# Kernel optimization log

Hardware: AMD Instinct MI355X
Metric: run time of the kernel (lower is better)

## Reference

```python
import jax, jax.numpy as jnp
import numpy as np

LOG_2PI = float(np.log(2.0 * np.pi))


def setup_inputs() -> dict:
    key = jax.random.key(0)
    k1, k2, k3 = jax.random.split(key, 3)
    B, T, F, K = 16, 1024, 1024, 500
    X = jax.random.normal(k1, (B, T, F), dtype=jnp.float32)
    mu = jax.random.normal(k2, (K, F), dtype=jnp.float32)
    # cov must be positive for log(cov); uniform in [0.5, 1.5)
    cov = jax.random.uniform(k3, (K, F), dtype=jnp.float32) + 0.5
    return {"X": X, "mu": mu, "cov": cov}


def reference(X, mu, cov):
    # Diagonal-covariance GMM log-likelihoods: out[b,t,k] = log N(X[b,t]; mu[k], diag(cov[k]))
    # Algebraic expansion of 0.5*sum((x-mu)^2/cov) into two GEMMs + bias, avoiding
    # the BxTxKxF broadcast intermediate. Same math as the torch module.
    D = mu.shape[-1]
    inv_cov = 1.0 / cov                                   # (K, F)
    C = -0.5 * D * LOG_2PI - 0.5 * jnp.sum(jnp.log(cov), axis=-1)  # (K,)
    quad = jnp.einsum('btf,kf->btk', X * X, inv_cov)      # sum x^2/cov
    cross = jnp.einsum('btf,kf->btk', X, mu * inv_cov)    # sum x*mu/cov
    const = jnp.sum(mu * mu * inv_cov, axis=-1)           # (K,) sum mu^2/cov
    ULL = 0.5 * (quad - 2.0 * cross + const[None, None, :])
    return C[None, None, :] - ULL                         # (B, T, K)
```

## Files before the change

### kernel.cpp

```cpp
#include <hip/hip_runtime.h>
#include <hip/hip_bf16.h>


typedef __attribute__((ext_vector_type(8))) __bf16 bf16x8;
typedef __attribute__((ext_vector_type(4))) float  f32x4;

#define LOG_2PI 1.837877066409345339082f

constexpr int M_TOT = 16384;
constexpr int F_DIM = 1024;
constexpr int K_GMM = 500;
constexpr int N_PAD = 512;

constexpr int BM  = 128;
constexpr int BN  = 128;
constexpr int BKF = 32;
constexpr int NIT = F_DIM / BKF;

__device__ __forceinline__ void gload_lds16(const void* g, void* l) {
    __builtin_amdgcn_global_load_lds(
        (const __attribute__((address_space(1))) unsigned*)g,
        (__attribute__((address_space(3))) unsigned*)l, 16, 0, 0);
}

__device__ __forceinline__ unsigned pack_sq_x(float x) {
    __hip_bfloat162 h = __float22bfloat162_rn(make_float2(x * x, x));
    union { __hip_bfloat162 h; unsigned u; } cv;
    cv.h = h;
    return cv.u;
}

__global__ __launch_bounds__(256) void prep_w_kernel(
    const float* __restrict__ mu, const float* __restrict__ cov,
    unsigned* __restrict__ Wimg, float* __restrict__ bias)
{
    const int k = blockIdx.x;
    const int t = threadIdx.x;
    const int r  = k & 127;
    const int tt = k >> 7;
    const int rsw = r & 7;
    float sl = 0.f, sq = 0.f;
    #pragma unroll
    for (int j = 0; j < 4; ++j) {
        const int f  = t + j * 256;
        const int it = f >> 5;
        const int cc = (f >> 2) & 7;
        const int q  = f & 3;
        const int dw = (tt * 32 + it) * 4096 + r * 32 + ((cc ^ rsw) << 2) + q;
        if (k < K_GMM) {
            const float c = cov[k * F_DIM + f];
            const float m = mu[k * F_DIM + f];
            const float ic = 1.0f / c;
            __hip_bfloat162 h = __float22bfloat162_rn(make_float2(-0.5f * ic, m * ic));
            union { __hip_bfloat162 h; unsigned u; } cv; cv.h = h;
            Wimg[dw] = cv.u;
            sl += logf(c);
            sq += m * m * ic;
        } else {
            Wimg[dw] = 0u;
        }
    }
    #pragma unroll
    for (int off = 32; off > 0; off >>= 1) {
        sl += __shfl_down(sl, off, 64);
        sq += __shfl_down(sq, off, 64);
    }
    __shared__ float red[8];
    if ((t & 63) == 0) { red[(t >> 6) * 2] = sl; red[(t >> 6) * 2 + 1] = sq; }
    __syncthreads();
    if (t == 0) {
        const float SL = red[0] + red[2] + red[4] + red[6];
        const float SQ = red[1] + red[3] + red[5] + red[7];
        bias[k] = (k < K_GMM)
                ? (-0.5f * (F_DIM * LOG_2PI) - 0.5f * SL - 0.5f * SQ) : 0.f;
    }
}

__global__ __launch_bounds__(256, 2) void gemm_kernel(
    const float* __restrict__ X, const unsigned* __restrict__ Wimg,
    const float* __restrict__ bias, float* __restrict__ out)
{
    __shared__ __align__(16) char smem[65536];
    float* ep = reinterpret_cast<float*>(smem);

    const int bid    = blockIdx.x;
    const int m_base = (bid & 127) * BM;
    const int n_tile = bid >> 7;
    const int n_base = n_tile * BN;

    const int tid  = threadIdx.x;
    const int lane = tid & 63;
    const int wv   = tid >> 6;
    const int wr   = (wv >> 1) * 64;
    const int wc   = (wv & 1) * 64;
    const int hi   = lane >> 4;
    const int lo   = lane & 15;
    const int lsw  = lo & 7;

    const int sr = tid >> 1;
    const int sh = tid & 1;

    const float4* Xv   = reinterpret_cast<const float4*>(X);
    const char*   Wimc = reinterpret_cast<const char*>(Wimg);

    f32x4 acc[4][4];
    #pragma unroll
    for (int a = 0; a < 4; ++a)
        #pragma unroll
        for (int b = 0; b < 4; ++b)
            acc[a][b] = (f32x4){0.f, 0.f, 0.f, 0.f};

    {
        const char* g0 = Wimc + (size_t)(n_tile * 32 + 0) * 16384;
        #pragma unroll
        for (int i = 0; i < 4; ++i)
            gload_lds16(g0 + i * 4096 + wv * 1024 + lane * 16,
                        smem + 32768 + i * 4096 + wv * 1024);
        float4 a0[4];
        #pragma unroll
        for (int j = 0; j < 4; ++j)
            a0[j] = Xv[(m_base + sr) * (F_DIM / 4) + sh * 4 + j];
        unsigned short* A0 = reinterpret_cast<unsigned short*>(smem);
        #pragma unroll
        for (int j = 0; j < 4; ++j) {
            const int chunk = (sh * 4 + j) ^ (sr & 7);
            uint4 wa;
            wa.x = pack_sq_x(a0[j].x);
            wa.y = pack_sq_x(a0[j].y);
            wa.z = pack_sq_x(a0[j].z);
            wa.w = pack_sq_x(a0[j].w);
            *reinterpret_cast<uint4*>(&A0[sr * 64 + chunk * 8]) = wa;
        }
    }
    __syncthreads();

    for (int it = 0; it < NIT; ++it) {
        const int cur = it & 1;
        const int nxt = cur ^ 1;
        const unsigned short* Asc =
            reinterpret_cast<const unsigned short*>(smem + cur * 16384);
        const unsigned short* Bsc =
            reinterpret_cast<const unsigned short*>(smem + 32768 + cur * 16384);
        char*           Bdst = smem + 32768 + nxt * 16384;
        unsigned short* Adst = reinterpret_cast<unsigned short*>(smem + nxt * 16384);

        float4 a_next[4];
        if (it + 1 < NIT) {
            const char* gs = Wimc + (size_t)(n_tile * 32 + it + 1) * 16384;
            #pragma unroll
            for (int i = 0; i < 4; ++i)
                gload_lds16(gs + i * 4096 + wv * 1024 + lane * 16,
                            Bdst + i * 4096 + wv * 1024);
            #pragma unroll
            for (int j = 0; j < 4; ++j)
                a_next[j] = Xv[(m_base + sr) * (F_DIM / 4) + (it + 1) * 8 + sh * 4 + j];
        }

        #pragma unroll
        for (int c = 0; c < 2; ++c) {
            bf16x8 af[4], bf[4];
            #pragma unroll
            for (int a = 0; a < 4; ++a) {
                const int row   = wr + a * 16 + lo;
                const int chunk = (c * 4 + hi) ^ lsw;
                af[a] = *reinterpret_cast<const bf16x8*>(&Asc[row * 64 + chunk * 8]);
            }
            #pragma unroll
            for (int b = 0; b < 4; ++b) {
                const int row   = wc + b * 16 + lo;
                const int chunk = (c * 4 + hi) ^ lsw;
                bf[b] = *reinterpret_cast<const bf16x8*>(&Bsc[row * 64 + chunk * 8]);
            }
            #pragma unroll
            for (int a = 0; a < 4; ++a)
                #pragma unroll
                for (int b = 0; b < 4; ++b)
                    acc[a][b] = __builtin_amdgcn_mfma_f32_16x16x32_bf16(
                        af[a], bf[b], acc[a][b], 0, 0, 0);
        }

        if (it + 1 < NIT) {
            #pragma unroll
            for (int j = 0; j < 4; ++j) {
                const int chunk = (sh * 4 + j) ^ (sr & 7);
                uint4 wa;
                wa.x = pack_sq_x(a_next[j].x);
                wa.y = pack_sq_x(a_next[j].y);
                wa.z = pack_sq_x(a_next[j].z);
                wa.w = pack_sq_x(a_next[j].w);
                *reinterpret_cast<uint4*>(&Adst[sr * 64 + chunk * 8]) = wa;
            }
        }
        __syncthreads();
    }

    const int ncols = (K_GMM - n_base < BN) ? (K_GMM - n_base) : BN;
    #pragma unroll
    for (int p = 0; p < 2; ++p) {
        __syncthreads();
        if ((wv >> 1) == p) {
            #pragma unroll
            for (int b = 0; b < 4; ++b) {
                const int col = wc + b * 16 + lo;
                const float bv = bias[n_base + col];
                #pragma unroll
                for (int a = 0; a < 4; ++a)
                    #pragma unroll
                    for (int i = 0; i < 4; ++i)
                        ep[(a * 16 + hi * 4 + i) * 128 + col] = acc[a][b][i] + bv;
            }
        }
        __syncthreads();
        #pragma unroll
        for (int k = 0; k < 8; ++k) {
            const int f    = k * 256 + tid;
            const int row  = f >> 5;
            const int slot = f & 31;
            if (slot * 4 < ncols) {
                const float4 v = *reinterpret_cast<const float4*>(&ep[row * 128 + slot * 4]);
                *reinterpret_cast<float4*>(
                    &out[(size_t)(m_base + p * 64 + row) * K_GMM + n_base + slot * 4]) = v;
            }
        }
    }
}

extern "C" void kernel_launch(void* const* d_in, const int* in_sizes, int n_in,
                              void* d_out, int out_size, void* d_ws, size_t ws_size,
                              hipStream_t stream)
{
    (void)in_sizes; (void)n_in; (void)out_size; (void)ws_size;
    const float* X   = (const float*)d_in[0];
    const float* mu  = (const float*)d_in[1];
    const float* cov = (const float*)d_in[2];
    float* out = (float*)d_out;

    unsigned* Wimg = (unsigned*)d_ws;
    float*    bias = (float*)((char*)d_ws + (size_t)N_PAD * F_DIM * 4);

    prep_w_kernel<<<dim3(N_PAD), dim3(256), 0, stream>>>(mu, cov, Wimg, bias);
    gemm_kernel<<<dim3((M_TOT / BM) * (N_PAD / BN)), dim3(256), 0, stream>>>(X, Wimg, bias, out);
}
```

Baseline: 57.82 us.

## Deepen GEMM pipeline with triple-buffered B tiles and explicit waitcnt barriers

The GEMM main loop is restructured so the weight tiles are triple-buffered in LDS (80KB) and prefetched two iterations ahead. X rows alternate between two register buffers, and the loop is unrolled by two. The implicit __syncthreads is replaced by manual s_waitcnt vmcnt(8)/lgkmcnt(0) plus s_barrier and sched_barrier, which lets one stage's loads stay in flight across the barrier. The aim is to hide global-load latency better; the cost is more LDS per block and fragile hand-counted waitcnt logic.

New measurement: 54.60 us. 1.06x faster.

```diff
diff --git a/kernel.cpp b/kernel.cpp
--- a/kernel.cpp
+++ b/kernel.cpp
@@ -80,7 +80,7 @@
     const float* __restrict__ X, const unsigned* __restrict__ Wimg,
     const float* __restrict__ bias, float* __restrict__ out)
 {
-    __shared__ __align__(16) char smem[65536];
+    __shared__ __align__(16) char smem[81920];
     float* ep = reinterpret_cast<float*>(smem);
 
     const int bid    = blockIdx.x;
@@ -110,52 +110,36 @@
         for (int b = 0; b < 4; ++b)
             acc[a][b] = (f32x4){0.f, 0.f, 0.f, 0.f};
 
-    {
-        const char* g0 = Wimc + (size_t)(n_tile * 32 + 0) * 16384;
+    auto stageB = [&](int itS, int bufS) {
+        const char* gs = Wimc + (size_t)(n_tile * 32 + itS) * 16384;
         #pragma unroll
         for (int i = 0; i < 4; ++i)
-            gload_lds16(g0 + i * 4096 + wv * 1024 + lane * 16,
-                        smem + 32768 + i * 4096 + wv * 1024);
-        float4 a0[4];
+            gload_lds16(gs + i * 4096 + wv * 1024 + lane * 16,
+                        smem + 32768 + bufS * 16384 + i * 4096 + wv * 1024);
+    };
+    auto loadA = [&](int itS, float4* ar) {
         #pragma unroll
         for (int j = 0; j < 4; ++j)
-            a0[j] = Xv[(m_base + sr) * (F_DIM / 4) + sh * 4 + j];
-        unsigned short* A0 = reinterpret_cast<unsigned short*>(smem);
+            ar[j] = Xv[(m_base + sr) * (F_DIM / 4) + itS * 8 + sh * 4 + j];
+    };
+    auto packA = [&](const float4* ar, int ab) {
+        unsigned short* Ad = reinterpret_cast<unsigned short*>(smem + ab * 16384);
         #pragma unroll
         for (int j = 0; j < 4; ++j) {
             const int chunk = (sh * 4 + j) ^ (sr & 7);
             uint4 wa;
-            wa.x = pack_sq_x(a0[j].x);
-            wa.y = pack_sq_x(a0[j].y);
-            wa.z = pack_sq_x(a0[j].z);
-            wa.w = pack_sq_x(a0[j].w);
-            *reinterpret_cast<uint4*>(&A0[sr * 64 + chunk * 8]) = wa;
-        }
-    }
-    __syncthreads();
-
-    for (int it = 0; it < NIT; ++it) {
-        const int cur = it & 1;
-        const int nxt = cur ^ 1;
+            wa.x = pack_sq_x(ar[j].x);
+            wa.y = pack_sq_x(ar[j].y);
+            wa.z = pack_sq_x(ar[j].z);
+            wa.w = pack_sq_x(ar[j].w);
+            *reinterpret_cast<uint4*>(&Ad[sr * 64 + chunk * 8]) = wa;
+        }
+    };
+    auto compute = [&](int ab, int bb) {
         const unsigned short* Asc =
-            reinterpret_cast<const unsigned short*>(smem + cur * 16384);
+            reinterpret_cast<const unsigned short*>(smem + ab * 16384);
         const unsigned short* Bsc =
-            reinterpret_cast<const unsigned short*>(smem + 32768 + cur * 16384);
-        char*           Bdst = smem + 32768 + nxt * 16384;
-        unsigned short* Adst = reinterpret_cast<unsigned short*>(smem + nxt * 16384);
-
-        float4 a_next[4];
-        if (it + 1 < NIT) {
-            const char* gs = Wimc + (size_t)(n_tile * 32 + it + 1) * 16384;
-            #pragma unroll
-            for (int i = 0; i < 4; ++i)
-                gload_lds16(gs + i * 4096 + wv * 1024 + lane * 16,
-                            Bdst + i * 4096 + wv * 1024);
-            #pragma unroll
-            for (int j = 0; j < 4; ++j)
-                a_next[j] = Xv[(m_base + sr) * (F_DIM / 4) + (it + 1) * 8 + sh * 4 + j];
-        }
-
+            reinterpret_cast<const unsigned short*>(smem + 32768 + bb * 16384);
         #pragma unroll
         for (int c = 0; c < 2; ++c) {
             bf16x8 af[4], bf[4];
@@ -178,26 +162,49 @@
                     acc[a][b] = __builtin_amdgcn_mfma_f32_16x16x32_bf16(
                         af[a], bf[b], acc[a][b], 0, 0, 0);
         }
-
-        if (it + 1 < NIT) {
-            #pragma unroll
-            for (int j = 0; j < 4; ++j) {
-                const int chunk = (sh * 4 + j) ^ (sr & 7);
-                uint4 wa;
-                wa.x = pack_sq_x(a_next[j].x);
-                wa.y = pack_sq_x(a_next[j].y);
-                wa.z = pack_sq_x(a_next[j].z);
-                wa.w = pack_sq_x(a_next[j].w);
-                *reinterpret_cast<uint4*>(&Adst[sr * 64 + chunk * 8]) = wa;
-            }
-        }
-        __syncthreads();
+    };
+
+    float4 aA[4], aB[4];
+    stageB(0, 0);
+    loadA(0, aB);
+    stageB(1, 1);
+    loadA(1, aA);
+    packA(aB, 0);
+    asm volatile("s_waitcnt vmcnt(8) lgkmcnt(0)" ::: "memory");
+    __builtin_amdgcn_s_barrier();
+    __builtin_amdgcn_sched_barrier(0);
+
+    for (int it = 0; it < NIT; it += 2) {
+        const int b0 = it % 3;
+        const int b1 = (it + 1) % 3;
+        const int b2 = (it + 2) % 3;
+        const int b3 = (it + 3) % 3;
+
+        if (it + 2 < NIT) { stageB(it + 2, b2); loadA(it + 2, aB); }
+        compute(0, b0);
+        packA(aA, 1);
+        if (it + 2 < NIT)
+            asm volatile("s_waitcnt vmcnt(8) lgkmcnt(0)" ::: "memory");
+        else
+            asm volatile("s_waitcnt vmcnt(0) lgkmcnt(0)" ::: "memory");
+        __builtin_amdgcn_s_barrier();
+        __builtin_amdgcn_sched_barrier(0);
+
+        if (it + 3 < NIT) { stageB(it + 3, b3); loadA(it + 3, aA); }
+        compute(1, b1);
+        if (it + 2 < NIT) packA(aB, 0);
+        if (it + 3 < NIT)
+            asm volatile("s_waitcnt vmcnt(8) lgkmcnt(0)" ::: "memory");
+        else
+            asm volatile("s_waitcnt vmcnt(0) lgkmcnt(0)" ::: "memory");
+        __builtin_amdgcn_s_barrier();
+        __builtin_amdgcn_sched_barrier(0);
     }
 
     const int ncols = (K_GMM - n_base < BN) ? (K_GMM - n_base) : BN;
     #pragma unroll
     for (int p = 0; p < 2; ++p) {
-        __syncthreads();
+        if (p) __syncthreads();
         if ((wv >> 1) == p) {
             #pragma unroll
             for (int b = 0; b < 4; ++b) {
```
